# Performance work log

Hardware: AMD Instinct MI355X
Metric: run time of the kernel (lower is better)

The kernel has to match this reference:

```python
import jax, jax.numpy as jnp
from jax import lax
import numpy as np


def _farthest_point_sample(points, num_centroids):
    """points: [B, C, N] float. Returns int32 indices [B, num_centroids].

    Standard PointNet++ CUDA semantics: start from point index 0, maintain a
    running min squared distance to the selected set, pick argmax each step.
    """
    B, C, N = points.shape

    def step(carry, _):
        min_dist, farthest = carry  # [B, N], [B]
        # gather current centroid coords: [B, C, 1]
        centroid = jnp.take_along_axis(points, farthest[:, None, None], axis=2)
        d = jnp.sum((points - centroid) ** 2, axis=1)  # [B, N]
        min_dist = jnp.minimum(min_dist, d)
        nxt = jnp.argmax(min_dist, axis=1).astype(jnp.int32)  # [B]
        return (min_dist, nxt), farthest

    init = (jnp.full((B, N), jnp.finfo(points.dtype).max, points.dtype),
            jnp.zeros((B,), jnp.int32))
    _, idx = lax.scan(step, init, None, length=num_centroids)  # idx: [S, B]
    return idx.T  # [B, num_centroids]


def setup_inputs() -> dict:
    key = jax.random.key(0)
    B, C, N = 32, 3, 131072
    points = jax.random.normal(key, (B, C, N), dtype=jnp.float32)
    return {"points": points, "num_centroids": 2048}


def reference(points, num_centroids):
    return _farthest_point_sample(points, num_centroids)
```

## Files before the change

kernel.cpp:

```cpp
#include <hip/hip_runtime.h>
#include <stdint.h>

typedef unsigned long long u64;

#define NBATCH 32
#define NPTS   131072
#define KBLK   8
#define PPB    (NPTS / KBLK)
#define NTHR   1024
#define NWAVE  (NTHR / 64)
#define PPT    (PPB / NTHR)
#define FLT_MAX_C 3.402823466e+38f

__device__ __forceinline__ u64* slot_ptr(u64* slots, int b, int k, int par) {
    return slots + (((b * KBLK + k) << 1) | par);
}
__device__ __forceinline__ u64 ld_slot(const u64* p) {
    return __hip_atomic_load(p, __ATOMIC_RELAXED, __HIP_MEMORY_SCOPE_AGENT);
}

__global__ __launch_bounds__(NTHR, 4)
void fps_kernel(const float* __restrict__ points, int* __restrict__ out,
                u64* __restrict__ slots, int S)
{
    const int b    = blockIdx.x & (NBATCH - 1);
    const int kk   = blockIdx.x >> 5;
    const int t    = threadIdx.x;
    const int lane = t & 63;
    const int wv   = t >> 6;
    const int t4   = t * 4;

    const float* pb = points + (size_t)b * 3 * NPTS;
    const float* bx = pb + kk * PPB;
    const float* by = bx + NPTS;
    const float* bz = bx + 2 * NPTS;

    float px[PPT], py[PPT], pz[PPT], md[PPT];
#pragma unroll
    for (int c = 0; c < PPT / 4; ++c) {
        float4 vx = *(const float4*)(bx + c * (NTHR * 4) + t4);
        float4 vy = *(const float4*)(by + c * (NTHR * 4) + t4);
        float4 vz = *(const float4*)(bz + c * (NTHR * 4) + t4);
        px[c*4+0]=vx.x; px[c*4+1]=vx.y; px[c*4+2]=vx.z; px[c*4+3]=vx.w;
        py[c*4+0]=vy.x; py[c*4+1]=vy.y; py[c*4+2]=vy.z; py[c*4+3]=vy.w;
        pz[c*4+0]=vz.x; pz[c*4+1]=vz.y; pz[c*4+2]=vz.z; pz[c*4+3]=vz.w;
        md[c*4+0]=FLT_MAX_C; md[c*4+1]=FLT_MAX_C;
        md[c*4+2]=FLT_MAX_C; md[c*4+3]=FLT_MAX_C;
    }

    __shared__ u64   s_wk[NWAVE];
    __shared__ float s_bcf[4];

    float cx = pb[0], cy = pb[NPTS], cz = pb[2 * NPTS];
    if (kk == 0 && t == 0) out[(size_t)b * S] = 0;

    for (int s = 1; s < S; ++s) {
        float bestv = -1.0f;
        int   bestp = 0;
#pragma unroll
        for (int p = 0; p < PPT; ++p) {
            float dx = __fsub_rn(px[p], cx);
            float dy = __fsub_rn(py[p], cy);
            float dz = __fsub_rn(pz[p], cz);
            float d  = __fadd_rn(__fadd_rn(__fmul_rn(dx, dx), __fmul_rn(dy, dy)),
                                 __fmul_rn(dz, dz));
            float m  = fminf(md[p], d);
            md[p] = m;
            bool tk = m > bestv;
            bestv = tk ? m : bestv;
            bestp = tk ? p : bestp;
        }
        int gidx = kk * PPB + (bestp >> 2) * (NTHR * 4) + t4 + (bestp & 3);

        float bv = bestv; int bi = gidx;
#pragma unroll
        for (int off = 32; off >= 1; off >>= 1) {
            float ov = __shfl_down(bv, off);
            int   oi = __shfl_down(bi, off);
            bool tk = (ov > bv) || (ov == bv && oi < bi);
            bv = tk ? ov : bv;
            bi = tk ? oi : bi;
        }
        if (lane == 0)
            s_wk[wv] = ((u64)__float_as_uint(bv) << 17)
                     | (u64)(unsigned)(131071 - bi);
        __syncthreads();

        if (wv == 0) {
            u64 orig = (lane < NWAVE) ? s_wk[lane] : 0ull;
            u64 kmax = orig;
#pragma unroll
            for (int off = 8; off >= 1; off >>= 1) {
                u64 o = (u64)__shfl_xor((long long)kmax, off);
                kmax = (o > kmax) ? o : kmax;
            }
            u64 mydi = ((u64)(unsigned)s << 49) | kmax;
            if (lane == 0)
                (void)__hip_atomic_exchange(slot_ptr(slots, b, kk, s & 1),
                                            mydi, __ATOMIC_RELAXED,
                                            __HIP_MEMORY_SCOPE_AGENT);

            u64  got = 0;
            float gx = 0.f, gy = 0.f, gz = 0.f;
            bool pend = (lane < KBLK);
            if (lane == kk) {
                got = mydi; pend = false;
                int i0 = 131071 - (int)(mydi & 0x1FFFF);
                gx = pb[i0]; gy = pb[NPTS + i0]; gz = pb[2 * NPTS + i0];
            }
            u64* ps = slot_ptr(slots, b, lane & 7, s & 1);
            u64 a = pend ? ld_slot(ps) : 0ull;
            while (__ballot(pend)) {
                u64 nx = pend ? ld_slot(ps) : 0ull;
                if (pend && (int)(a >> 49) == s) {
                    got = a; pend = false;
                    int ii = 131071 - (int)(a & 0x1FFFF);
                    gx = pb[ii]; gy = pb[NPTS + ii]; gz = pb[2 * NPTS + ii];
                }
                a = nx;
            }

            u64 win = (lane < KBLK) ? got : 0ull;
#pragma unroll
            for (int off = 4; off >= 1; off >>= 1) {
                u64 o = (u64)__shfl_xor((long long)win, off);
                win = (o > win) ? o : win;
            }
            u64 bm = __ballot(lane < KBLK && got == win);
            int w  = __ffsll(bm) - 1;
            float cxn = __shfl(gx, w);
            float cyn = __shfl(gy, w);
            float czn = __shfl(gz, w);
            int idx = 131071 - (int)(win & 0x1FFFF);
            if (lane == 0) {
                s_bcf[0] = cxn; s_bcf[1] = cyn; s_bcf[2] = czn;
                if (kk == 0) out[(size_t)b * S + s] = idx;
            }
        }
        __syncthreads();
        cx = s_bcf[0];
        cy = s_bcf[1];
        cz = s_bcf[2];
    }
}

extern "C" void kernel_launch(void* const* d_in, const int* in_sizes, int n_in,
                              void* d_out, int out_size, void* d_ws, size_t ws_size,
                              hipStream_t stream) {
    const float* points = (const float*)d_in[0];
    int* out   = (int*)d_out;
    u64* slots = (u64*)d_ws;
    int S = out_size / NBATCH;
    fps_kernel<<<dim3(NBATCH * KBLK), dim3(NTHR), 0, stream>>>(points, out, slots, S);
}
```

Measured before the change: 5.960 ms.

## Have every wave poll cross-block slots to drop second block barrier

```diff
diff --git a/kernel.cpp b/kernel.cpp
--- a/kernel.cpp
+++ b/kernel.cpp
@@ -48,13 +48,13 @@
         md[c*4+2]=FLT_MAX_C; md[c*4+3]=FLT_MAX_C;
     }
 
-    __shared__ u64   s_wk[NWAVE];
-    __shared__ float s_bcf[4];
+    __shared__ u64 s_wk[2][NWAVE];
 
     float cx = pb[0], cy = pb[NPTS], cz = pb[2 * NPTS];
     if (kk == 0 && t == 0) out[(size_t)b * S] = 0;
 
     for (int s = 1; s < S; ++s) {
+        const int par = s & 1;
         float bestv = -1.0f;
         int   bestp = 0;
 #pragma unroll
@@ -82,65 +82,57 @@
             bi = tk ? oi : bi;
         }
         if (lane == 0)
-            s_wk[wv] = ((u64)__float_as_uint(bv) << 17)
-                     | (u64)(unsigned)(131071 - bi);
+            s_wk[par][wv] = ((u64)__float_as_uint(bv) << 17)
+                          | (u64)(unsigned)(131071 - bi);
         __syncthreads();
 
-        if (wv == 0) {
-            u64 orig = (lane < NWAVE) ? s_wk[lane] : 0ull;
-            u64 kmax = orig;
+        u64 orig = (lane < NWAVE) ? s_wk[par][lane] : 0ull;
+        u64 kmax = orig;
 #pragma unroll
-            for (int off = 8; off >= 1; off >>= 1) {
-                u64 o = (u64)__shfl_xor((long long)kmax, off);
-                kmax = (o > kmax) ? o : kmax;
+        for (int off = 8; off >= 1; off >>= 1) {
+            u64 o = (u64)__shfl_xor((long long)kmax, off);
+            kmax = (o > kmax) ? o : kmax;
+        }
+        u64 mydi = ((u64)(unsigned)s << 49) | kmax;
+        if (t == 0)
+            (void)__hip_atomic_exchange(slot_ptr(slots, b, kk, par),
+                                        mydi, __ATOMIC_RELAXED,
+                                        __HIP_MEMORY_SCOPE_AGENT);
+
+        u64  got = 0;
+        float gx = 0.f, gy = 0.f, gz = 0.f;
+        bool pend = (lane < KBLK);
+        if (lane == kk) {
+            got = mydi; pend = false;
+            int i0 = 131071 - (int)(mydi & 0x1FFFF);
+            gx = pb[i0]; gy = pb[NPTS + i0]; gz = pb[2 * NPTS + i0];
+        }
+        u64* ps = slot_ptr(slots, b, lane & (KBLK - 1), par);
+        u64 a = pend ? ld_slot(ps) : 0ull;
+        while (__ballot(pend)) {
+            u64 nx = pend ? ld_slot(ps) : 0ull;
+            if (pend && (int)(a >> 49) == s) {
+                got = a; pend = false;
+                int ii = 131071 - (int)(a & 0x1FFFF);
+                gx = pb[ii]; gy = pb[NPTS + ii]; gz = pb[2 * NPTS + ii];
             }
-            u64 mydi = ((u64)(unsigned)s << 49) | kmax;
-            if (lane == 0)
-                (void)__hip_atomic_exchange(slot_ptr(slots, b, kk, s & 1),
-                                            mydi, __ATOMIC_RELAXED,
-                                            __HIP_MEMORY_SCOPE_AGENT);
+            a = nx;
+        }
 
-            u64  got = 0;
-            float gx = 0.f, gy = 0.f, gz = 0.f;
-            bool pend = (lane < KBLK);
-            if (lane == kk) {
-                got = mydi; pend = false;
-                int i0 = 131071 - (int)(mydi & 0x1FFFF);
-                gx = pb[i0]; gy = pb[NPTS + i0]; gz = pb[2 * NPTS + i0];
-            }
-            u64* ps = slot_ptr(slots, b, lane & 7, s & 1);
-            u64 a = pend ? ld_slot(ps) : 0ull;
-            while (__ballot(pend)) {
-                u64 nx = pend ? ld_slot(ps) : 0ull;
-                if (pend && (int)(a >> 49) == s) {
-                    got = a; pend = false;
-                    int ii = 131071 - (int)(a & 0x1FFFF);
-                    gx = pb[ii]; gy = pb[NPTS + ii]; gz = pb[2 * NPTS + ii];
-                }
-                a = nx;
-            }
-
-            u64 win = (lane < KBLK) ? got : 0ull;
+        u64 wn = (lane < KBLK) ? got : 0ull;
 #pragma unroll
-            for (int off = 4; off >= 1; off >>= 1) {
-                u64 o = (u64)__shfl_xor((long long)win, off);
-                win = (o > win) ? o : win;
-            }
-            u64 bm = __ballot(lane < KBLK && got == win);
-            int w  = __ffsll(bm) - 1;
-            float cxn = __shfl(gx, w);
-            float cyn = __shfl(gy, w);
-            float czn = __shfl(gz, w);
-            int idx = 131071 - (int)(win & 0x1FFFF);
-            if (lane == 0) {
-                s_bcf[0] = cxn; s_bcf[1] = cyn; s_bcf[2] = czn;
-                if (kk == 0) out[(size_t)b * S + s] = idx;
-            }
+        for (int off = 4; off >= 1; off >>= 1) {
+            u64 o = (u64)__shfl_xor((long long)wn, off);
+            wn = (o > wn) ? o : wn;
         }
-        __syncthreads();
-        cx = s_bcf[0];
-        cy = s_bcf[1];
-        cz = s_bcf[2];
+        u64 win = (u64)__shfl((long long)wn, 0);
+        u64 bm = __ballot(lane < KBLK && got == win);
+        int w  = __ffsll(bm) - 1;
+        cx = __shfl(gx, w);
+        cy = __shfl(gy, w);
+        cz = __shfl(gz, w);
+        if (kk == 0 && t == 0)
+            out[(size_t)b * S + s] = 131071 - (int)(win & 0x1FFFF);
     }
 }
 
```

After: 6.528 ms. 9.5% more time.
